# Kernel optimization log

Hardware: AMD Instinct MI355X
Metric: run time of the kernel (lower is better)

Reference implementation:

```python
import jax, jax.numpy as jnp
import numpy as np

N_NODES = 200_000
N_EDGES = 6_400_000
N_GRAPHS = 2048
VOCAB = 10_000
EMB = 64
HID = 64
NUM_CLASSES = 2


def setup_inputs() -> dict:
    key = jax.random.key(0)
    ks = jax.random.split(key, 12)
    x = jax.random.randint(ks[0], (N_NODES,), 0, VOCAB)
    edge_index = jax.random.randint(ks[1], (2, N_EDGES), 0, N_NODES)
    batch = jnp.sort(jax.random.randint(ks[2], (N_NODES,), 0, N_GRAPHS))
    s = 0.05
    return {
        "x": x,
        "edge_index": edge_index,
        "batch": batch,
        "emb": jax.random.normal(ks[3], (VOCAB, EMB), jnp.float32) * s,
        "W1_l": jax.random.normal(ks[4], (HID, EMB), jnp.float32) * s,
        "b1": jnp.zeros((HID,), jnp.float32),
        "W1_r": jax.random.normal(ks[5], (HID, EMB), jnp.float32) * s,
        "W2_l": jax.random.normal(ks[6], (HID, HID), jnp.float32) * s,
        "b2": jnp.zeros((HID,), jnp.float32),
        "W2_r": jax.random.normal(ks[7], (HID, HID), jnp.float32) * s,
        "Wout": jax.random.normal(ks[8], (NUM_CLASSES, HID), jnp.float32) * s,
        "bout": jnp.zeros((NUM_CLASSES,), jnp.float32),
    }


def _sage_conv(h, src, dst, W_l, b, W_r):
    # mean-aggregate messages from src at dst (PyG SAGEConv, aggr='mean')
    msg_sum = jax.ops.segment_sum(h[src], dst, num_segments=N_NODES)
    cnt = jax.ops.segment_sum(jnp.ones((src.shape[0], 1), h.dtype), dst,
                              num_segments=N_NODES)
    mean = msg_sum / jnp.maximum(cnt, 1.0)  # zero-degree nodes -> 0
    # out = lin_l(mean_neighbors) + lin_r(x); lin_r has no bias in PyG
    return mean @ W_l.T + b + h @ W_r.T


def reference(x, edge_index, batch, emb, W1_l, b1, W1_r, W2_l, b2, W2_r,
              Wout, bout):
    src, dst = edge_index[0], edge_index[1]
    h = emb[x]  # [N, EMB]
    h = jax.nn.relu(_sage_conv(h, src, dst, W1_l, b1, W1_r))
    h = jax.nn.relu(_sage_conv(h, src, dst, W2_l, b2, W2_r))
    # global_mean_pool over graph ids
    pooled = jax.ops.segment_sum(h, batch, num_segments=N_GRAPHS)
    cnt = jax.ops.segment_sum(jnp.ones((h.shape[0], 1), h.dtype), batch,
                              num_segments=N_GRAPHS)
    pooled = pooled / jnp.maximum(cnt, 1.0)
    return pooled @ Wout.T + bout  # [N_GRAPHS, NUM_CLASSES]
```

## Files before the change

### kernel.cpp

```cpp
#include <hip/hip_runtime.h>
#include <hip/hip_fp16.h>
#include <stdint.h>


#define NPB 4
#define NBUCK 256
#define TILE 4096
#define EPT 16
#define MAXN 1024

typedef __attribute__((ext_vector_type(8))) _Float16 half8;
typedef __attribute__((ext_vector_type(4))) float f32x4;

__device__ __forceinline__ int bucket_of(int dstv, int n_nodes) {
  return (int)(((unsigned)dstv * 256u) / (unsigned)n_nodes);
}

__device__ __forceinline__ void acc8h(float* a, uint4 u, float m) {
  const __half2* hp = (const __half2*)&u;
#pragma unroll
  for (int q = 0; q < 4; ++q) {
    float2 f = __half22float2(hp[q]);
    a[2 * q]     = fmaf(m, f.x, a[2 * q]);
    a[2 * q + 1] = fmaf(m, f.y, a[2 * q + 1]);
  }
}

__device__ __forceinline__ void add8(float* a, uint4 u) {
  const __half2* hp = (const __half2*)&u;
#pragma unroll
  for (int q = 0; q < 4; ++q) {
    float2 f = __half22float2(hp[q]);
    a[2 * q]     += f.x;
    a[2 * q + 1] += f.y;
  }
}

__global__ void k_init(int* __restrict__ gcur, int cap) {
  gcur[threadIdx.x] = threadIdx.x * cap;
}

__global__ void k_part(const int* __restrict__ src, const int* __restrict__ dst,
                       int* __restrict__ gcur, unsigned* __restrict__ pairs,
                       int n_edges, int n_nodes, int chunk) {
  __shared__ int hist[NBUCK * 4];
  __shared__ int base[NBUCK * 4];
  int t = threadIdx.x;
  int g = t >> 6;
  int beg = blockIdx.x * chunk;
  int end = min(beg + chunk, n_edges);
  for (int tbeg = beg; tbeg < end; tbeg += TILE) {
    int cnt = min(TILE, end - tbeg);
    hist[t] = 0; hist[t + 256] = 0; hist[t + 512] = 0; hist[t + 768] = 0;
    __syncthreads();
    unsigned pk[EPT];
    int r[EPT], bk[EPT];
    bool v[EPT];
#pragma unroll
    for (int k = 0; k < EPT; ++k) {
      int li = k * 256 + t;
      v[k] = li < cnt;
      if (v[k]) {
        int i = tbeg + li;
        int s = src[i];
        int d = dst[i];
        bk[k] = bucket_of(d, n_nodes);
        unsigned nb0 = ((unsigned)bk[k] * (unsigned)n_nodes + 255u) >> 8;
        pk[k] = (((unsigned)d - nb0) << 18) | (unsigned)s;
        r[k] = atomicAdd(&hist[bk[k] * 4 + g], 1);
      }
    }
    __syncthreads();
    int h0 = hist[t * 4 + 0], h1 = hist[t * 4 + 1];
    int h2 = hist[t * 4 + 2], h3 = hist[t * 4 + 3];
    int tot = h0 + h1 + h2 + h3;
    int b0 = (tot > 0) ? atomicAdd(&gcur[t], tot) : 0;
    base[t * 4 + 0] = b0;
    base[t * 4 + 1] = b0 + h0;
    base[t * 4 + 2] = b0 + h0 + h1;
    base[t * 4 + 3] = b0 + h0 + h1 + h2;
    __syncthreads();
#pragma unroll
    for (int k = 0; k < EPT; ++k)
      if (v[k]) pairs[base[bk[k] * 4 + g] + r[k]] = pk[k];
    __syncthreads();
  }
}

__global__ void k_bscan2(const int* __restrict__ gcur, int* __restrict__ bbase,
                         int cap, int n_edges) {
  __shared__ int s[NBUCK];
  int t = threadIdx.x;
  s[t] = gcur[t] - t * cap;
  __syncthreads();
  for (int off = 1; off < NBUCK; off <<= 1) {
    int add = (t >= off) ? s[t - off] : 0;
    __syncthreads();
    s[t] += add;
    __syncthreads();
  }
  bbase[t] = (t == 0) ? 0 : s[t - 1];
  if (t == NBUCK - 1) bbase[NBUCK] = n_edges;
}

__global__ void k_bucket(const unsigned* __restrict__ pairs, const int* __restrict__ gcur,
                         const int* __restrict__ bbase, const int* __restrict__ x,
                         int* __restrict__ offs, unsigned* __restrict__ idx,
                         int n_nodes, int n_edges, int cap) {
  __shared__ int lcnt[MAXN];
  __shared__ int lcur[MAXN];
  __shared__ int stmp[256];
  int b = blockIdx.x, t = threadIdx.x;
  int nb0 = (int)((((unsigned)b * (unsigned)n_nodes) + 255u) >> 8);
  int nb1 = (int)((((unsigned)(b + 1) * (unsigned)n_nodes) + 255u) >> 8);
  if (nb1 > n_nodes) nb1 = n_nodes;
  int nn = nb1 - nb0;
  int rbeg = b * cap;
  int rend = gcur[b];
  int obase = bbase[b];
  for (int i = t; i < nn; i += 256) lcnt[i] = 0;
  __syncthreads();
  for (int i = rbeg + t; i < rend; i += 256)
    atomicAdd(&lcnt[pairs[i] >> 18], 1);
  __syncthreads();
  int i0 = t * 4;
  int v0 = (i0 + 0 < nn) ? lcnt[i0 + 0] : 0;
  int v1 = (i0 + 1 < nn) ? lcnt[i0 + 1] : 0;
  int v2 = (i0 + 2 < nn) ? lcnt[i0 + 2] : 0;
  int v3 = (i0 + 3 < nn) ? lcnt[i0 + 3] : 0;
  stmp[t] = v0 + v1 + v2 + v3;
  __syncthreads();
  for (int off = 1; off < 256; off <<= 1) {
    int add = (t >= off) ? stmp[t - off] : 0;
    __syncthreads();
    stmp[t] += add;
    __syncthreads();
  }
  int run = obase + ((t == 0) ? 0 : stmp[t - 1]);
  if (i0 + 0 < nn) { lcur[i0 + 0] = run; offs[nb0 + i0 + 0] = run; run += v0; }
  if (i0 + 1 < nn) { lcur[i0 + 1] = run; offs[nb0 + i0 + 1] = run; run += v1; }
  if (i0 + 2 < nn) { lcur[i0 + 2] = run; offs[nb0 + i0 + 2] = run; run += v2; }
  if (i0 + 3 < nn) { lcur[i0 + 3] = run; offs[nb0 + i0 + 3] = run; run += v3; }
  if (b == NBUCK - 1 && t == 0) offs[n_nodes] = n_edges;
  __syncthreads();
  for (int i = rbeg + t; i < rend; i += 256) {
    unsigned e = pairs[i];
    int s = (int)(e & 0x3FFFFu);
    int pos = atomicAdd(&lcur[e >> 18], 1);
    idx[pos] = ((unsigned)x[s] << 18) | (unsigned)s;
  }
}

__global__ void k_transpose4(const float* __restrict__ a0, const float* __restrict__ a1,
                             const float* __restrict__ a2, const float* __restrict__ a3,
                             float* __restrict__ wt) {
  const float* s = (blockIdx.x == 0) ? a0 : (blockIdx.x == 1) ? a1 : (blockIdx.x == 2) ? a2 : a3;
  float* d = wt + blockIdx.x * 4096;
  for (int i = threadIdx.x; i < 4096; i += blockDim.x) {
    int r = i >> 6, c = i & 63;
    d[c * 64 + r] = s[i];
  }
}

__global__ void k_packB(const float* __restrict__ W2l, const float* __restrict__ W2r,
                        __half* __restrict__ pB) {
  int i = blockIdx.x * 256 + threadIdx.x;
  if (i >= 8192) return;
  int j = i & 7, l = (i >> 3) & 63, kt = (i >> 9) & 1, nt = (i >> 10) & 3, mat = i >> 12;
  int k = kt * 32 + (l >> 4) * 8 + j;
  int n = nt * 16 + (l & 15);
  const float* W = mat ? W2r : W2l;
  pB[i] = __float2half(W[n * 64 + k]);
}

__global__ void k_prep(const float* __restrict__ emb, const float* __restrict__ w1lT,
                       const float* __restrict__ w1rT, const float* __restrict__ b1,
                       __half* __restrict__ te, float* __restrict__ trb, int vocab) {
  __shared__ float se[NPB][64];
  int wid = threadIdx.x >> 6, lane = threadIdx.x & 63;
  int v = blockIdx.x * NPB + wid;
  if (v >= vocab) return;
  se[wid][lane] = emb[(size_t)v * 64 + lane];
  __syncwarp();
  float aL = 0.f, aR = b1[lane];
#pragma unroll 8
  for (int f = 0; f < 64; ++f) {
    float ev = se[wid][f];
    aL = fmaf(ev, w1lT[f * 64 + lane], aL);
    aR = fmaf(ev, w1rT[f * 64 + lane], aR);
  }
  te[(size_t)v * 64 + lane] = __float2half(aL);
  trb[(size_t)v * 64 + lane] = aR;
}

__global__ __launch_bounds__(64, 6) void
k_gather1(const unsigned* __restrict__ idx, const int* __restrict__ offs,
          const __half* __restrict__ te, const float* __restrict__ trb,
          const int* __restrict__ x, __half* __restrict__ h1, int n_nodes) {
  int lane = threadIdx.x;
  int r8 = lane >> 3, s8 = (lane & 7) << 3;
  int node = blockIdx.x;
  if (node >= n_nodes) return;
  int xv = x[node];
  int beg = offs[node], end = offs[node + 1];
  float a[8];
#pragma unroll
  for (int q = 0; q < 8; ++q) a[q] = 0.f;
  for (int c = beg; c < end; c += 64) {
    int nit = min(end - c, 64);
    unsigned eidx = idx[c + min(lane, nit - 1)];
    int ngrp = (nit + 7) >> 3;
    int nfg = nit >> 3;
    uint4 u0, u1, u2, u3, u4, u5, u6, u7;
#define CLD1(J) if (J < ngrp) { \
      int vv = (int)(__shfl(eidx, min(J * 8 + r8, nit - 1)) >> 18); \
      u##J = *(const uint4*)(te + ((size_t)vv << 6) + s8); }
    CLD1(0) CLD1(1) CLD1(2) CLD1(3) CLD1(4) CLD1(5) CLD1(6) CLD1(7)
#undef CLD1
#define CACC1(J) if (J < nfg) add8(a, u##J); \
    else if (J < ngrp) acc8h(a, u##J, (J * 8 + r8 < nit) ? 1.f : 0.f);
    CACC1(0) CACC1(1) CACC1(2) CACC1(3) CACC1(4) CACC1(5) CACC1(6) CACC1(7)
#undef CACC1
  }
  float4 t0, t1;
  if (lane < 8) {
    const float* tp = trb + ((size_t)xv << 6) + s8;
    t0 = *(const float4*)tp;
    t1 = *(const float4*)(tp + 4);
  }
#pragma unroll
  for (int q = 0; q < 8; ++q) {
    a[q] += __shfl_xor(a[q], 8);
    a[q] += __shfl_xor(a[q], 16);
    a[q] += __shfl_xor(a[q], 32);
  }
  int deg = end - beg;
  float inv = (deg > 0) ? 1.f / (float)deg : 0.f;
  if (lane < 8) {
    __half hh[8];
    hh[0] = __float2half(fmaxf(fmaf(a[0], inv, t0.x), 0.f));
    hh[1] = __float2half(fmaxf(fmaf(a[1], inv, t0.y), 0.f));
    hh[2] = __float2half(fmaxf(fmaf(a[2], inv, t0.z), 0.f));
    hh[3] = __float2half(fmaxf(fmaf(a[3], inv, t0.w), 0.f));
    hh[4] = __float2half(fmaxf(fmaf(a[4], inv, t1.x), 0.f));
    hh[5] = __float2half(fmaxf(fmaf(a[5], inv, t1.y), 0.f));
    hh[6] = __float2half(fmaxf(fmaf(a[6], inv, t1.z), 0.f));
    hh[7] = __float2half(fmaxf(fmaf(a[7], inv, t1.w), 0.f));
    *(uint4*)(h1 + ((size_t)node << 6) + s8) = *(uint4*)hh;
  }
}

__global__ __launch_bounds__(64) void
k_gemm(const __half* __restrict__ h1, const __half* __restrict__ pB,
       const float* __restrict__ b2, __half* __restrict__ g1,
       float* __restrict__ s1, int n_nodes) {
  int lane = threadIdx.x;
  int nbase = blockIdx.x * 16;
  int row = lane & 15, grp = lane >> 4;
  const half8 a0 = *(const half8*)(h1 + ((size_t)(nbase + row) << 6) + grp * 8);
  const half8 a1 = *(const half8*)(h1 + ((size_t)(nbase + row) << 6) + 32 + grp * 8);
#pragma unroll
  for (int t = 0; t < 8; ++t) {
    const half8 b0 = *(const half8*)(pB + (t * 2 + 0) * 512 + lane * 8);
    const half8 b1 = *(const half8*)(pB + (t * 2 + 1) * 512 + lane * 8);
    f32x4 acc = {0.f, 0.f, 0.f, 0.f};
    acc = __builtin_amdgcn_mfma_f32_16x16x32_f16(a0, b0, acc, 0, 0, 0);
    acc = __builtin_amdgcn_mfma_f32_16x16x32_f16(a1, b1, acc, 0, 0, 0);
    int out = (t & 3) * 16 + (lane & 15);
    if (t < 4) {
#pragma unroll
      for (int r = 0; r < 4; ++r) {
        int node = nbase + grp * 4 + r;
        if (node < n_nodes) g1[((size_t)node << 6) + out] = __float2half(acc[r]);
      }
    } else {
      float bias = b2[out];
#pragma unroll
      for (int r = 0; r < 4; ++r) {
        int node = nbase + grp * 4 + r;
        if (node < n_nodes) s1[((size_t)node << 6) + out] = acc[r] + bias;
      }
    }
  }
}

__global__ __launch_bounds__(64, 6) void
k_conv2(const unsigned* __restrict__ idx, const int* __restrict__ offs,
        const __half* __restrict__ g1, const float* __restrict__ s1,
        const float* __restrict__ wout, float* __restrict__ o, int n_nodes) {
  __shared__ float sm[64];
  int lane = threadIdx.x;
  int r8 = lane >> 3, s8 = (lane & 7) << 3;
  int node = blockIdx.x;
  if (node >= n_nodes) return;
  float s1v = s1[((size_t)node << 6) + lane];
  float w0 = wout[lane], w1v = wout[64 + lane];
  int beg = offs[node], end = offs[node + 1];
  float a[8];
#pragma unroll
  for (int q = 0; q < 8; ++q) a[q] = 0.f;
  for (int c = beg; c < end; c += 64) {
    int nit = min(end - c, 64);
    unsigned eidx = idx[c + min(lane, nit - 1)];
    int ngrp = (nit + 7) >> 3;
    int nfg = nit >> 3;
    uint4 u0, u1, u2, u3, u4, u5, u6, u7;
#define CLD2(J) if (J < ngrp) { \
      int vv = (int)(__shfl(eidx, min(J * 8 + r8, nit - 1)) & 0x3FFFFu); \
      u##J = *(const uint4*)(g1 + ((size_t)vv << 6) + s8); }
    CLD2(0) CLD2(1) CLD2(2) CLD2(3) CLD2(4) CLD2(5) CLD2(6) CLD2(7)
#undef CLD2
#define CACC2(J) if (J < nfg) add8(a, u##J); \
    else if (J < ngrp) acc8h(a, u##J, (J * 8 + r8 < nit) ? 1.f : 0.f);
    CACC2(0) CACC2(1) CACC2(2) CACC2(3) CACC2(4) CACC2(5) CACC2(6) CACC2(7)
#undef CACC2
  }
#pragma unroll
  for (int q = 0; q < 8; ++q) {
    a[q] += __shfl_xor(a[q], 8);
    a[q] += __shfl_xor(a[q], 16);
    a[q] += __shfl_xor(a[q], 32);
  }
  int deg = end - beg;
  float inv = (deg > 0) ? 1.f / (float)deg : 0.f;
  if (lane < 8) {
#pragma unroll
    for (int q = 0; q < 8; ++q) sm[s8 + q] = a[q] * inv;
  }
  __syncthreads();
  float h2 = fmaxf(sm[lane] + s1v, 0.f);
  float p0 = h2 * w0;
  float p1 = h2 * w1v;
  for (int off = 32; off > 0; off >>= 1) {
    p0 += __shfl_down(p0, off);
    p1 += __shfl_down(p1, off);
  }
  if (lane == 0) {
    o[((size_t)node << 1) + 0] = p0;
    o[((size_t)node << 1) + 1] = p1;
  }
}

__global__ void k_goffs(const int* __restrict__ batch, int* __restrict__ goffs,
                        int n_nodes, int n_graphs) {
  int i = blockIdx.x * blockDim.x + threadIdx.x;
  if (i >= n_nodes) return;
  int b = batch[i];
  int bp = (i == 0) ? -1 : batch[i - 1];
  for (int g = bp + 1; g <= b; ++g) goffs[g] = i;
  if (i == n_nodes - 1)
    for (int g = b + 1; g <= n_graphs; ++g) goffs[g] = n_nodes;
}

__global__ void k_pool(const float2* __restrict__ o, const int* __restrict__ goffs,
                       const float* __restrict__ bout, float* __restrict__ out,
                       int n_graphs) {
  int wid = threadIdx.x >> 6, lane = threadIdx.x & 63;
  int g = blockIdx.x * NPB + wid;
  if (g >= n_graphs) return;
  int beg = goffs[g], end = goffs[g + 1];
  float a0 = 0.f, a1 = 0.f;
  for (int n = beg + lane; n < end; n += 64) {
    float2 v = o[n];
    a0 += v.x;
    a1 += v.y;
  }
  for (int off = 32; off > 0; off >>= 1) {
    a0 += __shfl_down(a0, off);
    a1 += __shfl_down(a1, off);
  }
  if (lane == 0) {
    int cnt = end - beg;
    float inv = (cnt > 0) ? 1.f / (float)cnt : 0.f;
    out[g * 2 + 0] = a0 * inv + bout[0];
    out[g * 2 + 1] = a1 * inv + bout[1];
  }
}

extern "C" void kernel_launch(void* const* d_in, const int* in_sizes, int n_in,
                              void* d_out, int out_size, void* d_ws, size_t ws_size,
                              hipStream_t stream) {
  const int* x = (const int*)d_in[0];
  const int* ei = (const int*)d_in[1];
  const int* batch = (const int*)d_in[2];
  const float* emb = (const float*)d_in[3];
  const float* W1l = (const float*)d_in[4];
  const float* b1 = (const float*)d_in[5];
  const float* W1r = (const float*)d_in[6];
  const float* W2l = (const float*)d_in[7];
  const float* b2 = (const float*)d_in[8];
  const float* W2r = (const float*)d_in[9];
  const float* Wout = (const float*)d_in[10];
  const float* bout = (const float*)d_in[11];
  float* out = (float*)d_out;

  int n_nodes = in_sizes[0];
  int n_edges = in_sizes[1] / 2;
  int vocab = in_sizes[3] / 64;
  int n_graphs = out_size / 2;
  const int* src = ei;
  const int* dst = ei + n_edges;

  int cap = n_edges / NBUCK + n_edges / (NBUCK * 8) + 1024;
  int ntiles = (n_nodes + 15) / 16;

  char* p = (char*)d_ws;
  auto alloc = [&](size_t bytes) -> void* {
    void* r = (void*)p;
    p += (bytes + 255) & ~(size_t)255;
    return r;
  };
  __half* te = (__half*)alloc((size_t)vocab * 64 * 2);
  float* trb = (float*)alloc((size_t)vocab * 64 * 4);
  float* wt = (float*)alloc(2 * 4096 * 4);
  __half* pB = (__half*)alloc(8192 * 2);
  int* offs = (int*)alloc((size_t)(n_nodes + 1) * 4);
  int* goffs = (int*)alloc((size_t)(n_graphs + 1) * 4);
  int* bbase = (int*)alloc((NBUCK + 1) * 4);
  int* gcur = (int*)alloc(NBUCK * 4);
  unsigned* idx = (unsigned*)alloc((size_t)n_edges * 4);
  __half* h1 = (__half*)alloc((size_t)(ntiles * 16) * 64 * 2);
  size_t pairs_bytes = (size_t)NBUCK * cap * 4;
  size_t g1_bytes = (size_t)n_nodes * 64 * 2;
  unsigned* pairs = (unsigned*)alloc(pairs_bytes > g1_bytes ? pairs_bytes : g1_bytes);
  float* s1 = (float*)alloc((size_t)n_nodes * 64 * 4);
  float* o = (float*)alloc((size_t)n_nodes * 2 * 4);
  __half* g1 = (__half*)pairs;

  k_init<<<1, NBUCK, 0, stream>>>(gcur, cap);
  k_transpose4<<<2, 256, 0, stream>>>(W1l, W1r, W1l, W1l, wt);
  k_prep<<<(vocab + NPB - 1) / NPB, 64 * NPB, 0, stream>>>(emb, wt, wt + 4096, b1, te, trb, vocab);
  k_packB<<<32, 256, 0, stream>>>(W2l, W2r, pB);

  int part_blocks = 512;
  int chunk = (n_edges + part_blocks - 1) / part_blocks;
  k_part<<<part_blocks, 256, 0, stream>>>(src, dst, gcur, pairs, n_edges, n_nodes, chunk);
  k_bscan2<<<1, NBUCK, 0, stream>>>(gcur, bbase, cap, n_edges);
  k_bucket<<<NBUCK, 256, 0, stream>>>(pairs, gcur, bbase, x, offs, idx, n_nodes, n_edges, cap);

  k_goffs<<<(n_nodes + 255) / 256, 256, 0, stream>>>(batch, goffs, n_nodes, n_graphs);

  k_gather1<<<n_nodes, 64, 0, stream>>>(idx, offs, te, trb, x, h1, n_nodes);
  k_gemm<<<ntiles, 64, 0, stream>>>(h1, pB, b2, g1, s1, n_nodes);
  k_conv2<<<n_nodes, 64, 0, stream>>>(idx, offs, g1, s1, Wout, o, n_nodes);
  k_pool<<<(n_graphs + NPB - 1) / NPB, 64 * NPB, 0, stream>>>((const float2*)o, goffs, bout, out, n_graphs);
}
```

Before: 401.4 us.

## Process two nodes per wave in gathers and drop bucket scan kernels

The gather1 and conv2 kernels now handle two destination nodes per 64-thread block. Gathers for both nodes are interleaved so each wave keeps more memory loads in flight. The CSR offsets become separate begin/end arrays that index directly into the capacity-padded bucket regions, which removes the bucket-base scan kernel. The gcur init kernel is folded into packB. Launch bounds drop from 6 to 4 waves per SIMD to make room for the extra registers, and the idx buffer grows to the padded size.

```diff
diff --git a/kernel.cpp b/kernel.cpp
--- a/kernel.cpp
+++ b/kernel.cpp
@@ -34,10 +34,6 @@
     a[2 * q]     += f.x;
     a[2 * q + 1] += f.y;
   }
-}
-
-__global__ void k_init(int* __restrict__ gcur, int cap) {
-  gcur[threadIdx.x] = threadIdx.x * cap;
 }
 
 __global__ void k_part(const int* __restrict__ src, const int* __restrict__ dst,
@@ -87,26 +83,10 @@
   }
 }
 
-__global__ void k_bscan2(const int* __restrict__ gcur, int* __restrict__ bbase,
-                         int cap, int n_edges) {
-  __shared__ int s[NBUCK];
-  int t = threadIdx.x;
-  s[t] = gcur[t] - t * cap;
-  __syncthreads();
-  for (int off = 1; off < NBUCK; off <<= 1) {
-    int add = (t >= off) ? s[t - off] : 0;
-    __syncthreads();
-    s[t] += add;
-    __syncthreads();
-  }
-  bbase[t] = (t == 0) ? 0 : s[t - 1];
-  if (t == NBUCK - 1) bbase[NBUCK] = n_edges;
-}
-
 __global__ void k_bucket(const unsigned* __restrict__ pairs, const int* __restrict__ gcur,
-                         const int* __restrict__ bbase, const int* __restrict__ x,
-                         int* __restrict__ offs, unsigned* __restrict__ idx,
-                         int n_nodes, int n_edges, int cap) {
+                         const int* __restrict__ x, int* __restrict__ obeg,
+                         int* __restrict__ oend, unsigned* __restrict__ idx,
+                         int n_nodes, int cap) {
   __shared__ int lcnt[MAXN];
   __shared__ int lcur[MAXN];
   __shared__ int stmp[256];
@@ -117,7 +97,6 @@
   int nn = nb1 - nb0;
   int rbeg = b * cap;
   int rend = gcur[b];
-  int obase = bbase[b];
   for (int i = t; i < nn; i += 256) lcnt[i] = 0;
   __syncthreads();
   for (int i = rbeg + t; i < rend; i += 256)
@@ -136,12 +115,11 @@
     stmp[t] += add;
     __syncthreads();
   }
-  int run = obase + ((t == 0) ? 0 : stmp[t - 1]);
-  if (i0 + 0 < nn) { lcur[i0 + 0] = run; offs[nb0 + i0 + 0] = run; run += v0; }
-  if (i0 + 1 < nn) { lcur[i0 + 1] = run; offs[nb0 + i0 + 1] = run; run += v1; }
-  if (i0 + 2 < nn) { lcur[i0 + 2] = run; offs[nb0 + i0 + 2] = run; run += v2; }
-  if (i0 + 3 < nn) { lcur[i0 + 3] = run; offs[nb0 + i0 + 3] = run; run += v3; }
-  if (b == NBUCK - 1 && t == 0) offs[n_nodes] = n_edges;
+  int run = rbeg + ((t == 0) ? 0 : stmp[t - 1]);
+  if (i0 + 0 < nn) { lcur[i0 + 0] = run; obeg[nb0 + i0 + 0] = run; oend[nb0 + i0 + 0] = run + v0; run += v0; }
+  if (i0 + 1 < nn) { lcur[i0 + 1] = run; obeg[nb0 + i0 + 1] = run; oend[nb0 + i0 + 1] = run + v1; run += v1; }
+  if (i0 + 2 < nn) { lcur[i0 + 2] = run; obeg[nb0 + i0 + 2] = run; oend[nb0 + i0 + 2] = run + v2; run += v2; }
+  if (i0 + 3 < nn) { lcur[i0 + 3] = run; obeg[nb0 + i0 + 3] = run; oend[nb0 + i0 + 3] = run + v3; run += v3; }
   __syncthreads();
   for (int i = rbeg + t; i < rend; i += 256) {
     unsigned e = pairs[i];
@@ -163,7 +141,8 @@
 }
 
 __global__ void k_packB(const float* __restrict__ W2l, const float* __restrict__ W2r,
-                        __half* __restrict__ pB) {
+                        __half* __restrict__ pB, int* __restrict__ gcur, int cap) {
+  if (blockIdx.x == 0) gcur[threadIdx.x] = threadIdx.x * cap;
   int i = blockIdx.x * 256 + threadIdx.x;
   if (i >= 8192) return;
   int j = i & 7, l = (i >> 3) & 63, kt = (i >> 9) & 1, nt = (i >> 10) & 3, mat = i >> 12;
@@ -193,60 +172,99 @@
   trb[(size_t)v * 64 + lane] = aR;
 }
 
-__global__ __launch_bounds__(64, 6) void
-k_gather1(const unsigned* __restrict__ idx, const int* __restrict__ offs,
-          const __half* __restrict__ te, const float* __restrict__ trb,
-          const int* __restrict__ x, __half* __restrict__ h1, int n_nodes) {
+#define LDG(U, J, EIX, NIT, NG, TBL, OP) \
+  if (J < NG) { int vv = (int)(__shfl(EIX, min(J * 8 + r8, NIT - 1)) OP); \
+    U = *(const uint4*)(TBL + ((size_t)vv << 6) + s8); }
+#define ACG(U, J, NF, NG, NIT, ACC) \
+  if (J < NF) add8(ACC, U); \
+  else if (J < NG) acc8h(ACC, U, (J * 8 + r8 < NIT) ? 1.f : 0.f);
+
+__global__ __launch_bounds__(64, 4) void
+k_gather1(const unsigned* __restrict__ idx, const int* __restrict__ obeg,
+          const int* __restrict__ oend, const __half* __restrict__ te,
+          const float* __restrict__ trb, const int* __restrict__ x,
+          __half* __restrict__ h1, int n_nodes) {
   int lane = threadIdx.x;
   int r8 = lane >> 3, s8 = (lane & 7) << 3;
-  int node = blockIdx.x;
-  if (node >= n_nodes) return;
-  int xv = x[node];
-  int beg = offs[node], end = offs[node + 1];
-  float a[8];
-#pragma unroll
-  for (int q = 0; q < 8; ++q) a[q] = 0.f;
-  for (int c = beg; c < end; c += 64) {
-    int nit = min(end - c, 64);
-    unsigned eidx = idx[c + min(lane, nit - 1)];
-    int ngrp = (nit + 7) >> 3;
-    int nfg = nit >> 3;
-    uint4 u0, u1, u2, u3, u4, u5, u6, u7;
-#define CLD1(J) if (J < ngrp) { \
-      int vv = (int)(__shfl(eidx, min(J * 8 + r8, nit - 1)) >> 18); \
-      u##J = *(const uint4*)(te + ((size_t)vv << 6) + s8); }
-    CLD1(0) CLD1(1) CLD1(2) CLD1(3) CLD1(4) CLD1(5) CLD1(6) CLD1(7)
-#undef CLD1
-#define CACC1(J) if (J < nfg) add8(a, u##J); \
-    else if (J < ngrp) acc8h(a, u##J, (J * 8 + r8 < nit) ? 1.f : 0.f);
-    CACC1(0) CACC1(1) CACC1(2) CACC1(3) CACC1(4) CACC1(5) CACC1(6) CACC1(7)
-#undef CACC1
-  }
-  float4 t0, t1;
+  int n0 = blockIdx.x * 2;
+  int n1 = n0 + 1;
+  if (n0 >= n_nodes) return;
+  bool has1 = n1 < n_nodes;
+  int xv0 = x[n0];
+  int xv1 = has1 ? x[n1] : 0;
+  int b0 = obeg[n0], e0 = oend[n0];
+  int b1 = has1 ? obeg[n1] : 0, e1 = has1 ? oend[n1] : 0;
+  float a0[8], a1[8];
+#pragma unroll
+  for (int q = 0; q < 8; ++q) { a0[q] = 0.f; a1[q] = 0.f; }
+  int c0 = b0, c1 = b1;
+  while (c0 < e0 || c1 < e1) {
+    int nit0 = (c0 < e0) ? min(e0 - c0, 64) : 0;
+    int nit1 = (c1 < e1) ? min(e1 - c1, 64) : 0;
+    unsigned ei0 = 0, ei1 = 0;
+    if (nit0) ei0 = idx[c0 + min(lane, nit0 - 1)];
+    if (nit1) ei1 = idx[c1 + min(lane, nit1 - 1)];
+    int ng0 = (nit0 + 7) >> 3, nf0 = nit0 >> 3;
+    int ng1 = (nit1 + 7) >> 3, nf1 = nit1 >> 3;
+    uint4 uA0, uA1, uA2, uA3, uA4, uA5, uA6, uA7;
+    uint4 uB0, uB1, uB2, uB3, uB4, uB5, uB6, uB7;
+    LDG(uA0, 0, ei0, nit0, ng0, te, >> 18) LDG(uA1, 1, ei0, nit0, ng0, te, >> 18)
+    LDG(uA2, 2, ei0, nit0, ng0, te, >> 18) LDG(uA3, 3, ei0, nit0, ng0, te, >> 18)
+    LDG(uA4, 4, ei0, nit0, ng0, te, >> 18) LDG(uA5, 5, ei0, nit0, ng0, te, >> 18)
+    LDG(uA6, 6, ei0, nit0, ng0, te, >> 18) LDG(uA7, 7, ei0, nit0, ng0, te, >> 18)
+    LDG(uB0, 0, ei1, nit1, ng1, te, >> 18) LDG(uB1, 1, ei1, nit1, ng1, te, >> 18)
+    LDG(uB2, 2, ei1, nit1, ng1, te, >> 18) LDG(uB3, 3, ei1, nit1, ng1, te, >> 18)
+    LDG(uB4, 4, ei1, nit1, ng1, te, >> 18) LDG(uB5, 5, ei1, nit1, ng1, te, >> 18)
+    LDG(uB6, 6, ei1, nit1, ng1, te, >> 18) LDG(uB7, 7, ei1, nit1, ng1, te, >> 18)
+    ACG(uA0, 0, nf0, ng0, nit0, a0) ACG(uA1, 1, nf0, ng0, nit0, a0)
+    ACG(uA2, 2, nf0, ng0, nit0, a0) ACG(uA3, 3, nf0, ng0, nit0, a0)
+    ACG(uA4, 4, nf0, ng0, nit0, a0) ACG(uA5, 5, nf0, ng0, nit0, a0)
+    ACG(uA6, 6, nf0, ng0, nit0, a0) ACG(uA7, 7, nf0, ng0, nit0, a0)
+    ACG(uB0, 0, nf1, ng1, nit1, a1) ACG(uB1, 1, nf1, ng1, nit1, a1)
+    ACG(uB2, 2, nf1, ng1, nit1, a1) ACG(uB3, 3, nf1, ng1, nit1, a1)
+    ACG(uB4, 4, nf1, ng1, nit1, a1) ACG(uB5, 5, nf1, ng1, nit1, a1)
+    ACG(uB6, 6, nf1, ng1, nit1, a1) ACG(uB7, 7, nf1, ng1, nit1, a1)
+    c0 += 64; c1 += 64;
+  }
+  float4 t00, t01, t10, t11;
   if (lane < 8) {
-    const float* tp = trb + ((size_t)xv << 6) + s8;
-    t0 = *(const float4*)tp;
-    t1 = *(const float4*)(tp + 4);
+    const float* tp0 = trb + ((size_t)xv0 << 6) + s8;
+    t00 = *(const float4*)tp0;
+    t01 = *(const float4*)(tp0 + 4);
+    const float* tp1 = trb + ((size_t)xv1 << 6) + s8;
+    t10 = *(const float4*)tp1;
+    t11 = *(const float4*)(tp1 + 4);
   }
 #pragma unroll
   for (int q = 0; q < 8; ++q) {
-    a[q] += __shfl_xor(a[q], 8);
-    a[q] += __shfl_xor(a[q], 16);
-    a[q] += __shfl_xor(a[q], 32);
-  }
-  int deg = end - beg;
-  float inv = (deg > 0) ? 1.f / (float)deg : 0.f;
+    a0[q] += __shfl_xor(a0[q], 8);  a0[q] += __shfl_xor(a0[q], 16); a0[q] += __shfl_xor(a0[q], 32);
+    a1[q] += __shfl_xor(a1[q], 8);  a1[q] += __shfl_xor(a1[q], 16); a1[q] += __shfl_xor(a1[q], 32);
+  }
+  int d0 = e0 - b0, d1 = e1 - b1;
+  float inv0 = (d0 > 0) ? 1.f / (float)d0 : 0.f;
+  float inv1 = (d1 > 0) ? 1.f / (float)d1 : 0.f;
   if (lane < 8) {
     __half hh[8];
-    hh[0] = __float2half(fmaxf(fmaf(a[0], inv, t0.x), 0.f));
-    hh[1] = __float2half(fmaxf(fmaf(a[1], inv, t0.y), 0.f));
-    hh[2] = __float2half(fmaxf(fmaf(a[2], inv, t0.z), 0.f));
-    hh[3] = __float2half(fmaxf(fmaf(a[3], inv, t0.w), 0.f));
-    hh[4] = __float2half(fmaxf(fmaf(a[4], inv, t1.x), 0.f));
-    hh[5] = __float2half(fmaxf(fmaf(a[5], inv, t1.y), 0.f));
-    hh[6] = __float2half(fmaxf(fmaf(a[6], inv, t1.z), 0.f));
-    hh[7] = __float2half(fmaxf(fmaf(a[7], inv, t1.w), 0.f));
-    *(uint4*)(h1 + ((size_t)node << 6) + s8) = *(uint4*)hh;
+    hh[0] = __float2half(fmaxf(fmaf(a0[0], inv0, t00.x), 0.f));
+    hh[1] = __float2half(fmaxf(fmaf(a0[1], inv0, t00.y), 0.f));
+    hh[2] = __float2half(fmaxf(fmaf(a0[2], inv0, t00.z), 0.f));
+    hh[3] = __float2half(fmaxf(fmaf(a0[3], inv0, t00.w), 0.f));
+    hh[4] = __float2half(fmaxf(fmaf(a0[4], inv0, t01.x), 0.f));
+    hh[5] = __float2half(fmaxf(fmaf(a0[5], inv0, t01.y), 0.f));
+    hh[6] = __float2half(fmaxf(fmaf(a0[6], inv0, t01.z), 0.f));
+    hh[7] = __float2half(fmaxf(fmaf(a0[7], inv0, t01.w), 0.f));
+    *(uint4*)(h1 + ((size_t)n0 << 6) + s8) = *(uint4*)hh;
+    if (has1) {
+      hh[0] = __float2half(fmaxf(fmaf(a1[0], inv1, t10.x), 0.f));
+      hh[1] = __float2half(fmaxf(fmaf(a1[1], inv1, t10.y), 0.f));
+      hh[2] = __float2half(fmaxf(fmaf(a1[2], inv1, t10.z), 0.f));
+      hh[3] = __float2half(fmaxf(fmaf(a1[3], inv1, t10.w), 0.f));
+      hh[4] = __float2half(fmaxf(fmaf(a1[4], inv1, t11.x), 0.f));
+      hh[5] = __float2half(fmaxf(fmaf(a1[5], inv1, t11.y), 0.f));
+      hh[6] = __float2half(fmaxf(fmaf(a1[6], inv1, t11.z), 0.f));
+      hh[7] = __float2half(fmaxf(fmaf(a1[7], inv1, t11.w), 0.f));
+      *(uint4*)(h1 + ((size_t)n1 << 6) + s8) = *(uint4*)hh;
+    }
   }
 }
 
@@ -284,60 +302,88 @@
   }
 }
 
-__global__ __launch_bounds__(64, 6) void
-k_conv2(const unsigned* __restrict__ idx, const int* __restrict__ offs,
-        const __half* __restrict__ g1, const float* __restrict__ s1,
-        const float* __restrict__ wout, float* __restrict__ o, int n_nodes) {
-  __shared__ float sm[64];
+__global__ __launch_bounds__(64, 4) void
+k_conv2(const unsigned* __restrict__ idx, const int* __restrict__ obeg,
+        const int* __restrict__ oend, const __half* __restrict__ g1,
+        const float* __restrict__ s1, const float* __restrict__ wout,
+        float* __restrict__ o, int n_nodes) {
+  __shared__ float sm[2][64];
   int lane = threadIdx.x;
   int r8 = lane >> 3, s8 = (lane & 7) << 3;
-  int node = blockIdx.x;
-  if (node >= n_nodes) return;
-  float s1v = s1[((size_t)node << 6) + lane];
+  int n0 = blockIdx.x * 2;
+  int n1 = n0 + 1;
+  if (n0 >= n_nodes) return;
+  bool has1 = n1 < n_nodes;
+  float s1v0 = s1[((size_t)n0 << 6) + lane];
+  float s1v1 = has1 ? s1[((size_t)n1 << 6) + lane] : 0.f;
   float w0 = wout[lane], w1v = wout[64 + lane];
-  int beg = offs[node], end = offs[node + 1];
-  float a[8];
-#pragma unroll
-  for (int q = 0; q < 8; ++q) a[q] = 0.f;
-  for (int c = beg; c < end; c += 64) {
-    int nit = min(end - c, 64);
-    unsigned eidx = idx[c + min(lane, nit - 1)];
-    int ngrp = (nit + 7) >> 3;
-    int nfg = nit >> 3;
-    uint4 u0, u1, u2, u3, u4, u5, u6, u7;
-#define CLD2(J) if (J < ngrp) { \
-      int vv = (int)(__shfl(eidx, min(J * 8 + r8, nit - 1)) & 0x3FFFFu); \
-      u##J = *(const uint4*)(g1 + ((size_t)vv << 6) + s8); }
-    CLD2(0) CLD2(1) CLD2(2) CLD2(3) CLD2(4) CLD2(5) CLD2(6) CLD2(7)
-#undef CLD2
-#define CACC2(J) if (J < nfg) add8(a, u##J); \
-    else if (J < ngrp) acc8h(a, u##J, (J * 8 + r8 < nit) ? 1.f : 0.f);
-    CACC2(0) CACC2(1) CACC2(2) CACC2(3) CACC2(4) CACC2(5) CACC2(6) CACC2(7)
-#undef CACC2
+  int b0 = obeg[n0], e0 = oend[n0];
+  int b1 = has1 ? obeg[n1] : 0, e1 = has1 ? oend[n1] : 0;
+  float a0[8], a1[8];
+#pragma unroll
+  for (int q = 0; q < 8; ++q) { a0[q] = 0.f; a1[q] = 0.f; }
+  int c0 = b0, c1 = b1;
+  while (c0 < e0 || c1 < e1) {
+    int nit0 = (c0 < e0) ? min(e0 - c0, 64) : 0;
+    int nit1 = (c1 < e1) ? min(e1 - c1, 64) : 0;
+    unsigned ei0 = 0, ei1 = 0;
+    if (nit0) ei0 = idx[c0 + min(lane, nit0 - 1)];
+    if (nit1) ei1 = idx[c1 + min(lane, nit1 - 1)];
+    int ng0 = (nit0 + 7) >> 3, nf0 = nit0 >> 3;
+    int ng1 = (nit1 + 7) >> 3, nf1 = nit1 >> 3;
+    uint4 uA0, uA1, uA2, uA3, uA4, uA5, uA6, uA7;
+    uint4 uB0, uB1, uB2, uB3, uB4, uB5, uB6, uB7;
+    LDG(uA0, 0, ei0, nit0, ng0, g1, & 0x3FFFFu) LDG(uA1, 1, ei0, nit0, ng0, g1, & 0x3FFFFu)
+    LDG(uA2, 2, ei0, nit0, ng0, g1, & 0x3FFFFu) LDG(uA3, 3, ei0, nit0, ng0, g1, & 0x3FFFFu)
+    LDG(uA4, 4, ei0, nit0, ng0, g1, & 0x3FFFFu) LDG(uA5, 5, ei0, nit0, ng0, g1, & 0x3FFFFu)
+    LDG(uA6, 6, ei0, nit0, ng0, g1, & 0x3FFFFu) LDG(uA7, 7, ei0, nit0, ng0, g1, & 0x3FFFFu)
+    LDG(uB0, 0, ei1, nit1, ng1, g1, & 0x3FFFFu) LDG(uB1, 1, ei1, nit1, ng1, g1, & 0x3FFFFu)
+    LDG(uB2, 2, ei1, nit1, ng1, g1, & 0x3FFFFu) LDG(uB3, 3, ei1, nit1, ng1, g1, & 0x3FFFFu)
+    LDG(uB4, 4, ei1, nit1, ng1, g1, & 0x3FFFFu) LDG(uB5, 5, ei1, nit1, ng1, g1, & 0x3FFFFu)
+    LDG(uB6, 6, ei1, nit1, ng1, g1, & 0x3FFFFu) LDG(uB7, 7, ei1, nit1, ng1, g1, & 0x3FFFFu)
+    ACG(uA0, 0, nf0, ng0, nit0, a0) ACG(uA1, 1, nf0, ng0, nit0, a0)
+    ACG(uA2, 2, nf0, ng0, nit0, a0) ACG(uA3, 3, nf0, ng0, nit0, a0)
+    ACG(uA4, 4, nf0, ng0, nit0, a0) ACG(uA5, 5, nf0, ng0, nit0, a0)
+    ACG(uA6, 6, nf0, ng0, nit0, a0) ACG(uA7, 7, nf0, ng0, nit0, a0)
+    ACG(uB0, 0, nf1, ng1, nit1, a1) ACG(uB1, 1, nf1, ng1, nit1, a1)
+    ACG(uB2, 2, nf1, ng1, nit1, a1) ACG(uB3, 3, nf1, ng1, nit1, a1)
+    ACG(uB4, 4, nf1, ng1, nit1, a1) ACG(uB5, 5, nf1, ng1, nit1, a1)
+    ACG(uB6, 6, nf1, ng1, nit1, a1) ACG(uB7, 7, nf1, ng1, nit1, a1)
+    c0 += 64; c1 += 64;
   }
 #pragma unroll
   for (int q = 0; q < 8; ++q) {
-    a[q] += __shfl_xor(a[q], 8);
-    a[q] += __shfl_xor(a[q], 16);
-    a[q] += __shfl_xor(a[q], 32);
-  }
-  int deg = end - beg;
-  float inv = (deg > 0) ? 1.f / (float)deg : 0.f;
+    a0[q] += __shfl_xor(a0[q], 8);  a0[q] += __shfl_xor(a0[q], 16); a0[q] += __shfl_xor(a0[q], 32);
+    a1[q] += __shfl_xor(a1[q], 8);  a1[q] += __shfl_xor(a1[q], 16); a1[q] += __shfl_xor(a1[q], 32);
+  }
+  int d0 = e0 - b0, d1 = e1 - b1;
+  float inv0 = (d0 > 0) ? 1.f / (float)d0 : 0.f;
+  float inv1 = (d1 > 0) ? 1.f / (float)d1 : 0.f;
   if (lane < 8) {
 #pragma unroll
-    for (int q = 0; q < 8; ++q) sm[s8 + q] = a[q] * inv;
+    for (int q = 0; q < 8; ++q) {
+      sm[0][s8 + q] = a0[q] * inv0;
+      sm[1][s8 + q] = a1[q] * inv1;
+    }
   }
   __syncthreads();
-  float h2 = fmaxf(sm[lane] + s1v, 0.f);
-  float p0 = h2 * w0;
-  float p1 = h2 * w1v;
+  float h20 = fmaxf(sm[0][lane] + s1v0, 0.f);
+  float h21 = fmaxf(sm[1][lane] + s1v1, 0.f);
+  float p00 = h20 * w0, p01 = h20 * w1v;
+  float p10 = h21 * w0, p11 = h21 * w1v;
   for (int off = 32; off > 0; off >>= 1) {
-    p0 += __shfl_down(p0, off);
-    p1 += __shfl_down(p1, off);
+    p00 += __shfl_down(p00, off);
+    p01 += __shfl_down(p01, off);
+    p10 += __shfl_down(p10, off);
+    p11 += __shfl_down(p11, off);
   }
   if (lane == 0) {
-    o[((size_t)node << 1) + 0] = p0;
-    o[((size_t)node << 1) + 1] = p1;
+    o[((size_t)n0 << 1) + 0] = p00;
+    o[((size_t)n0 << 1) + 1] = p01;
+    if (has1) {
+      o[((size_t)n1 << 1) + 0] = p10;
+      o[((size_t)n1 << 1) + 1] = p11;
+    }
   }
 }
 
@@ -414,11 +460,11 @@
   float* trb = (float*)alloc((size_t)vocab * 64 * 4);
   float* wt = (float*)alloc(2 * 4096 * 4);
   __half* pB = (__half*)alloc(8192 * 2);
-  int* offs = (int*)alloc((size_t)(n_nodes + 1) * 4);
+  int* obeg = (int*)alloc((size_t)n_nodes * 4);
+  int* oend = (int*)alloc((size_t)n_nodes * 4);
   int* goffs = (int*)alloc((size_t)(n_graphs + 1) * 4);
-  int* bbase = (int*)alloc((NBUCK + 1) * 4);
   int* gcur = (int*)alloc(NBUCK * 4);
-  unsigned* idx = (unsigned*)alloc((size_t)n_edges * 4);
+  unsigned* idx = (unsigned*)alloc((size_t)NBUCK * cap * 4);
   __half* h1 = (__half*)alloc((size_t)(ntiles * 16) * 64 * 2);
   size_t pairs_bytes = (size_t)NBUCK * cap * 4;
   size_t g1_bytes = (size_t)n_nodes * 64 * 2;
@@ -427,21 +473,19 @@
   float* o = (float*)alloc((size_t)n_nodes * 2 * 4);
   __half* g1 = (__half*)pairs;
 
-  k_init<<<1, NBUCK, 0, stream>>>(gcur, cap);
+  k_packB<<<32, 256, 0, stream>>>(W2l, W2r, pB, gcur, cap);
   k_transpose4<<<2, 256, 0, stream>>>(W1l, W1r, W1l, W1l, wt);
   k_prep<<<(vocab + NPB - 1) / NPB, 64 * NPB, 0, stream>>>(emb, wt, wt + 4096, b1, te, trb, vocab);
-  k_packB<<<32, 256, 0, stream>>>(W2l, W2r, pB);
 
   int part_blocks = 512;
   int chunk = (n_edges + part_blocks - 1) / part_blocks;
   k_part<<<part_blocks, 256, 0, stream>>>(src, dst, gcur, pairs, n_edges, n_nodes, chunk);
-  k_bscan2<<<1, NBUCK, 0, stream>>>(gcur, bbase, cap, n_edges);
-  k_bucket<<<NBUCK, 256, 0, stream>>>(pairs, gcur, bbase, x, offs, idx, n_nodes, n_edges, cap);
+  k_bucket<<<NBUCK, 256, 0, stream>>>(pairs, gcur, x, obeg, oend, idx, n_nodes, cap);
 
   k_goffs<<<(n_nodes + 255) / 256, 256, 0, stream>>>(batch, goffs, n_nodes, n_graphs);
 
-  k_gather1<<<n_nodes, 64, 0, stream>>>(idx, offs, te, trb, x, h1, n_nodes);
+  k_gather1<<<(n_nodes + 1) / 2, 64, 0, stream>>>(idx, obeg, oend, te, trb, x, h1, n_nodes);
   k_gemm<<<ntiles, 64, 0, stream>>>(h1, pB, b2, g1, s1, n_nodes);
-  k_conv2<<<n_nodes, 64, 0, stream>>>(idx, offs, g1, s1, Wout, o, n_nodes);
+  k_conv2<<<(n_nodes + 1) / 2, 64, 0, stream>>>(idx, obeg, oend, g1, s1, Wout, o, n_nodes);
   k_pool<<<(n_graphs + NPB - 1) / NPB, 64 * NPB, 0, stream>>>((const float2*)o, goffs, bout, out, n_graphs);
 }
```

New measurement: 489.2 us. 1.22x slower.
